# Kernel optimization log

Hardware: AMD Instinct MI355X
Metric: run time of the kernel (lower is better)

Reference implementation:

```python
import jax, jax.numpy as jnp
import numpy as np
from jax import lax


def _layernorm(x, g, b, eps=1e-5):
    mu = x.mean(-1, keepdims=True)
    var = ((x - mu) ** 2).mean(-1, keepdims=True)
    return (x - mu) * lax.rsqrt(var + eps) * g + b


def _conv1d(x, w, b):
    # x: (B, T, Cin), w: (K, Cin, Cout) -> (B, T, Cout), SAME padding
    return lax.conv_general_dilated(x, w, (1,), 'SAME',
                                    dimension_numbers=('NWC', 'WIO', 'NWC')) + b


def _gated(x, wf, bf, wg, bg):
    return jax.nn.relu(_conv1d(x, wf, bf)) * jax.nn.sigmoid(_conv1d(x, wg, bg))


def setup_inputs() -> dict:
    key = jax.random.key(0)
    ks = iter(jax.random.split(key, 32))
    B, T, F, H = 32, 1024, 64, 768
    ch = H // 3
    d = {'x': jax.random.normal(next(ks), (B, T, F), jnp.float32)}
    for k in (3, 5, 7):
        d[f'conv{k}_wf'] = jax.random.normal(next(ks), (k, F, ch), jnp.float32) * 0.05
        d[f'conv{k}_bf'] = jnp.zeros((ch,), jnp.float32)
        d[f'conv{k}_wg'] = jax.random.normal(next(ks), (k, F, ch), jnp.float32) * 0.05
        d[f'conv{k}_bg'] = jnp.zeros((ch,), jnp.float32)
    d['conv_ln_g'] = jnp.ones((H,), jnp.float32)
    d['conv_ln_b'] = jnp.zeros((H,), jnp.float32)
    for name in ('gqa_wq', 'gqa_wk', 'gqa_wv', 'gqa_wp'):
        d[name] = jax.random.normal(next(ks), (2, H, H), jnp.float32) * 0.02
    d['gqa_bp'] = jnp.zeros((2, H), jnp.float32)
    d['gqa_ln_g'] = jnp.ones((2, H), jnp.float32)
    d['gqa_ln_b'] = jnp.zeros((2, H), jnp.float32)
    d['proj_w'] = jax.random.normal(next(ks), (2 * H, H), jnp.float32) * 0.02
    d['proj_b'] = jnp.zeros((H,), jnp.float32)
    d['proj_ln_g'] = jnp.ones((H,), jnp.float32)
    d['proj_ln_b'] = jnp.zeros((H,), jnp.float32)
    return d


def _gqa(h, wq, wk, wv, wp, bp, ln_g, ln_b, n_groups=4):
    B, T, H = h.shape
    G, D = n_groups, H // n_groups
    scale = D ** -0.5
    Q = (h @ wq).reshape(B, T, G, D)
    K = (h @ wk).reshape(B, T, G, D)
    V = (h @ wv).reshape(B, T, G, D)
    attn = jax.nn.softmax(jnp.einsum('bqgd,bkgd->bgqk', Q, K) * scale, axis=-1)
    out = jnp.einsum('bgqk,bkgd->bqgd', attn, V).reshape(B, T, H)
    return _layernorm(h + out @ wp + bp, ln_g, ln_b)


def reference(x, conv3_wf, conv3_bf, conv3_wg, conv3_bg,
              conv5_wf, conv5_bf, conv5_wg, conv5_bg,
              conv7_wf, conv7_bf, conv7_wg, conv7_bg,
              conv_ln_g, conv_ln_b,
              gqa_wq, gqa_wk, gqa_wv, gqa_wp, gqa_bp, gqa_ln_g, gqa_ln_b,
              proj_w, proj_b, proj_ln_g, proj_ln_b):
    # Multi-scale gated conv front end (SAME padding -> all branches length T)
    o3 = _gated(x, conv3_wf, conv3_bf, conv3_wg, conv3_bg)
    o5 = _gated(x, conv5_wf, conv5_bf, conv5_wg, conv5_bg)
    o7 = _gated(x, conv7_wf, conv7_bf, conv7_wg, conv7_bg)
    h = _layernorm(jnp.concatenate([o3, o5, o7], axis=-1), conv_ln_g, conv_ln_b)
    # Two GQA blocks
    for i in range(2):
        h = _gqa(h, gqa_wq[i], gqa_wk[i], gqa_wv[i], gqa_wp[i],
                 gqa_bp[i], gqa_ln_g[i], gqa_ln_b[i])
    # mean + population-std pooling over time
    m = h.mean(axis=1)
    s = jnp.sqrt(((h - m[:, None, :]) ** 2).mean(axis=1))
    z = jnp.concatenate([m, s], axis=-1) @ proj_w + proj_b
    return jax.nn.relu(_layernorm(z, proj_ln_g, proj_ln_b))
```

## Files before the change

### kernel.cpp

```cpp
#include <hip/hip_runtime.h>
#include <hip/hip_bf16.h>


constexpr int Bb = 32, Tt = 1024, Ff = 64, Hh = 768, Gg = 4, Dd = 192;
constexpr float EPS = 1e-5f;
constexpr int WKMAX = 448;

typedef __attribute__((ext_vector_type(8))) short short8;
typedef __attribute__((ext_vector_type(4))) float floatx4;

__device__ __forceinline__ void async_copy16(const void* g, void* l) {
  __builtin_amdgcn_global_load_lds(
      (const __attribute__((address_space(1))) unsigned int*)g,
      (__attribute__((address_space(3))) unsigned int*)l, 16, 0, 0);
}

__device__ __forceinline__ short bf16s(float f) {
  __hip_bfloat16 h = __float2bfloat16(f);
  return *(short*)&h;
}

__device__ __forceinline__ unsigned int pack_bf16(float lo, float hi) {
  return (unsigned int)(unsigned short)bf16s(lo) |
         ((unsigned int)(unsigned short)bf16s(hi) << 16);
}

__device__ __forceinline__ float2 block_reduce2(float a, float b, float* tmp) {
  int lane = threadIdx.x & 63, wid = threadIdx.x >> 6;
#pragma unroll
  for (int off = 32; off > 0; off >>= 1) {
    a += __shfl_down(a, off);
    b += __shfl_down(b, off);
  }
  if (lane == 0) { tmp[wid] = a; tmp[4 + wid] = b; }
  __syncthreads();
  if (threadIdx.x == 0) {
    tmp[0] = tmp[0] + tmp[1] + tmp[2] + tmp[3];
    tmp[4] = tmp[4] + tmp[5] + tmp[6] + tmp[7];
  }
  __syncthreads();
  float2 r; r.x = tmp[0]; r.y = tmp[4];
  return r;
}

__global__ __launch_bounds__(256) void wt_cast_kernel(
    const float* __restrict__ wq, const float* __restrict__ wk,
    const float* __restrict__ wv, const float* __restrict__ wp,
    __hip_bfloat16* __restrict__ wt) {
  const int z = blockIdx.z;
  const int m = z & 3, i = z >> 2;
  const float* src =
      (m == 0 ? wq : m == 1 ? wk : m == 2 ? wv : wp) + (size_t)i * Hh * Hh;
  const float sc = (m == 0) ? 0.0721687836f : 1.f;
  __shared__ float tile[32][33];
  const int n0 = blockIdx.x * 32, k0 = blockIdx.y * 32;
  const int tx = threadIdx.x & 31, ty = threadIdx.x >> 5;
#pragma unroll
  for (int r = 0; r < 4; r++)
    tile[ty + 8 * r][tx] = src[(size_t)(k0 + ty + 8 * r) * Hh + n0 + tx];
  __syncthreads();
#pragma unroll
  for (int r = 0; r < 4; r++)
    wt[((size_t)z * Hh + n0 + ty + 8 * r) * Hh + k0 + tx] =
        __float2bfloat16(tile[tx][ty + 8 * r] * sc);
}

__global__ __launch_bounds__(256) void wcv_cast_kernel(
    const float* __restrict__ wf3, const float* __restrict__ wg3,
    const float* __restrict__ wf5, const float* __restrict__ wg5,
    const float* __restrict__ wf7, const float* __restrict__ wg7,
    __hip_bfloat16* __restrict__ wcv) {
  int idx = blockIdx.x * 256 + threadIdx.x;
  if (idx >= 3 * 512 * WKMAX) return;
  int j = idx / (512 * WKMAX);
  int rem = idx - j * 512 * WKMAX;
  int n = rem / WKMAX, k = rem % WKMAX;
  int Kw = 3 + 2 * j;
  float v = 0.f;
  if (k < Kw * 64) {
    const float* src = (n < 256) ? (j == 0 ? wf3 : j == 1 ? wf5 : wf7)
                                 : (j == 0 ? wg3 : j == 1 ? wg5 : wg7);
    v = src[(size_t)k * 256 + (n & 255)];
  }
  wcv[idx] = __float2bfloat16(v);
}

__global__ __launch_bounds__(256) void x_cast_kernel(
    const float* __restrict__ x, short* __restrict__ x16, int n8) {
  int idx = blockIdx.x * 256 + threadIdx.x;
  if (idx >= n8) return;
  const float4 a = ((const float4*)x)[idx * 2];
  const float4 b = ((const float4*)x)[idx * 2 + 1];
  short8 o;
  o[0] = bf16s(a.x); o[1] = bf16s(a.y); o[2] = bf16s(a.z); o[3] = bf16s(a.w);
  o[4] = bf16s(b.x); o[5] = bf16s(b.y); o[6] = bf16s(b.z); o[7] = bf16s(b.w);
  ((short8*)x16)[idx] = o;
}

__global__ __launch_bounds__(256) void conv_gemm_kernel(
    const short* __restrict__ x16, const short* __restrict__ wcv,
    short* __restrict__ yraw, int b0) {
  __shared__ __align__(16) short Asl[128 * 72];
  __shared__ __align__(16) short Bsl[128 * 72];
  const int t0 = blockIdx.x * 128, n0 = blockIdx.y * 128;
  const int bl = blockIdx.z / 3, j = blockIdx.z % 3;
  const int Kw = 3 + 2 * j, pad = j + 1;
  const int bglob = b0 + bl;
  const short* wb = wcv + (size_t)j * 512 * WKMAX;
  const int tid = threadIdx.x;
  const int lane = tid & 63;
  const int w = tid >> 6, wm = w >> 1, wn = w & 1;
  const int lm = lane & 15, quad = lane >> 4;

  floatx4 acc[4][4];
#pragma unroll
  for (int i = 0; i < 4; i++)
#pragma unroll
    for (int jj = 0; jj < 4; jj++) acc[i][jj] = (floatx4)0.f;

  for (int kk = 0; kk < Kw; kk++) {
    __syncthreads();
#pragma unroll
    for (int it = 0; it < 4; it++) {
      int s = it * 256 + tid;
      int row = s >> 3, c8 = s & 7;
      int t = t0 + row + kk - pad;
      short8 av = (short8)0;
      if (t >= 0 && t < Tt)
        av = *(const short8*)&x16[((size_t)bglob * Tt + t) * Ff + c8 * 8];
      *(short8*)&Asl[row * 72 + c8 * 8] = av;
      short8 bv = *(const short8*)&wb[(size_t)(n0 + row) * WKMAX + kk * 64 +
                                      c8 * 8];
      *(short8*)&Bsl[row * 72 + c8 * 8] = bv;
    }
    __syncthreads();
#pragma unroll
    for (int ks = 0; ks < 2; ks++) {
      short8 a[4], b[4];
#pragma unroll
      for (int i = 0; i < 4; i++)
        a[i] = *(const short8*)&Asl[(wm * 64 + i * 16 + lm) * 72 + ks * 32 +
                                    quad * 8];
#pragma unroll
      for (int jj = 0; jj < 4; jj++)
        b[jj] = *(const short8*)&Bsl[(wn * 64 + jj * 16 + lm) * 72 + ks * 32 +
                                     quad * 8];
#pragma unroll
      for (int i = 0; i < 4; i++)
#pragma unroll
        for (int jj = 0; jj < 4; jj++)
          acc[i][jj] = __builtin_amdgcn_mfma_f32_16x16x32_bf16(a[i], b[jj],
                                                               acc[i][jj],
                                                               0, 0, 0);
    }
  }

  const int rbase = quad * 4;
#pragma unroll
  for (int i = 0; i < 4; i++)
#pragma unroll
    for (int jj = 0; jj < 4; jj++) {
      int mrow = t0 + wm * 64 + i * 16 + rbase;
      int ncol = n0 + wn * 64 + jj * 16 + lm;
#pragma unroll
      for (int r = 0; r < 4; r++)
        yraw[((size_t)bl * Tt + mrow + r) * 1536 + j * 512 + ncol] =
            bf16s(acc[i][jj][r]);
    }
}

__global__ __launch_bounds__(256) void gate_ln_kernel(
    const short* __restrict__ yraw, __hip_bfloat16* __restrict__ h16,
    const float* __restrict__ bf3, const float* __restrict__ bg3,
    const float* __restrict__ bf5, const float* __restrict__ bg5,
    const float* __restrict__ bf7, const float* __restrict__ bg7,
    const float* __restrict__ g, const float* __restrict__ bt) {
  __shared__ float red[8];
  const size_t row = blockIdx.x;
  float v[3], s = 0.f, ss = 0.f;
#pragma unroll
  for (int jj = 0; jj < 3; jj++) {
    int c = threadIdx.x + jj * 256;
    int br = c >> 8, cc = c & 255;
    const float* bfp = br == 0 ? bf3 : br == 1 ? bf5 : bf7;
    const float* bgp = br == 0 ? bg3 : br == 1 ? bg5 : bg7;
    __hip_bfloat16 rf = *(const __hip_bfloat16*)&yraw[row * 1536 + br * 512 + cc];
    __hip_bfloat16 rg =
        *(const __hip_bfloat16*)&yraw[row * 1536 + br * 512 + 256 + cc];
    float f = __bfloat162float(rf) + bfp[cc];
    float gt = __bfloat162float(rg) + bgp[cc];
    float a = f > 0.f ? f : 0.f;
    float t = a * (1.f / (1.f + __expf(-gt)));
    v[jj] = t; s += t; ss += t * t;
  }
  float2 r = block_reduce2(s, ss, red);
  float mu = r.x * (1.f / Hh);
  float var = r.y * (1.f / Hh) - mu * mu;
  float rs = rsqrtf(var + EPS);
#pragma unroll
  for (int jj = 0; jj < 3; jj++) {
    int c = threadIdx.x + jj * 256;
    float o = (v[jj] - mu) * rs * g[c] + bt[c];
    h16[row * Hh + c] = __float2bfloat16(o);
  }
}

__global__ __launch_bounds__(256) void res_ln_kernel(
    __hip_bfloat16* __restrict__ h16, const __hip_bfloat16* __restrict__ y,
    const float* __restrict__ bp, const float* __restrict__ g,
    const float* __restrict__ bt) {
  __shared__ float red[8];
  const size_t row = blockIdx.x;
  float v[3], s = 0.f, ss = 0.f;
#pragma unroll
  for (int jj = 0; jj < 3; jj++) {
    int c = threadIdx.x + jj * 256;
    float t = __bfloat162float(h16[row * Hh + c]) +
              __bfloat162float(y[row * Hh + c]) + bp[c];
    v[jj] = t; s += t; ss += t * t;
  }
  float2 r = block_reduce2(s, ss, red);
  float mu = r.x * (1.f / Hh);
  float var = r.y * (1.f / Hh) - mu * mu;
  float rs = rsqrtf(var + EPS);
#pragma unroll
  for (int jj = 0; jj < 3; jj++) {
    int c = threadIdx.x + jj * 256;
    float o = (v[jj] - mu) * rs * g[c] + bt[c];
    h16[row * Hh + c] = __float2bfloat16(o);
  }
}

template <int MODE>
__global__ __launch_bounds__(512, 2) void gemm_8ph(
    const short* __restrict__ A, const short* __restrict__ Bt,
    short* __restrict__ out_q, short* __restrict__ out_k,
    short* __restrict__ out_v) {
  constexpr int K = 768;
  constexpr int NT = K / 32;
  constexpr int NB = (MODE == 0) ? 9 : 3;
  __shared__ __align__(16) short lds[4][16384];

  const int nwg = gridDim.x;
  const int qq = nwg >> 3, rr = nwg & 7;
  const int xcd = blockIdx.x & 7, bidx = blockIdx.x >> 3;
  const int swz =
      (xcd < rr ? xcd * (qq + 1) : rr * (qq + 1) + (xcd - rr) * qq) + bidx;
  const int nb = swz % NB, mb = swz / NB;
  const int n0 = nb * 256, m0 = mb * 256;

  const int tid = threadIdx.x;
  const int lane = tid & 63, w = tid >> 6;
  const int lm = lane & 15, quad = lane >> 4;
  const int wm = w >> 2, wn = w & 3;

  const short* sA[2];
  const short* sB[2];
  int dst[2];
#pragma unroll
  for (int li = 0; li < 2; li++) {
    int l = li * 512 + tid;
    int reg = l >> 6, cs = l & 63;
    int cs2 = cs ^ (((cs >> 5) & 1) << 1);
    int row = (reg << 4) + (cs2 >> 2);
    int col = (cs2 & 3) << 3;
    sA[li] = A + (size_t)(m0 + row) * K + col;
    sB[li] = Bt + (size_t)(n0 + row) * K + col;
    dst[li] = l * 8;
  }

#define STAGE8(kt, ring)                                   \
  {                                                        \
    const int _o = (kt) * 32;                              \
    async_copy16(sA[0] + _o, &lds[ring][dst[0]]);          \
    async_copy16(sB[0] + _o, &lds[ring][8192 + dst[0]]);   \
    async_copy16(sA[1] + _o, &lds[ring][dst[1]]);          \
    async_copy16(sB[1] + _o, &lds[ring][8192 + dst[1]]);   \
  }

  const int lane_sh = (lm * 32 + quad * 8) ^ ((lm >> 3) << 4);

  floatx4 acc[8][4];
#pragma unroll
  for (int i = 0; i < 8; i++)
#pragma unroll
    for (int j = 0; j < 4; j++) acc[i][j] = (floatx4)0.f;

  STAGE8(0, 0);
  STAGE8(1, 1);
  STAGE8(2, 2);
  asm volatile("s_waitcnt vmcnt(8)" ::: "memory");
  asm volatile("s_barrier" ::: "memory");
  __builtin_amdgcn_sched_barrier(0);

  for (int t = 0; t < NT; t++) {
    const int ring = t & 3;
    if (t + 3 < NT) STAGE8(t + 3, (t + 3) & 3);

    short8 a[8], b[4];
#pragma unroll
    for (int i = 0; i < 8; i++)
      a[i] = *(const short8*)&lds[ring][(wm * 8 + i) * 512 + lane_sh];
#pragma unroll
    for (int j = 0; j < 4; j++)
      b[j] = *(const short8*)&lds[ring][8192 + (wn * 4 + j) * 512 + lane_sh];

    __builtin_amdgcn_s_setprio(1);
#pragma unroll
    for (int i = 0; i < 8; i++)
#pragma unroll
      for (int j = 0; j < 4; j++)
        acc[i][j] = __builtin_amdgcn_mfma_f32_16x16x32_bf16(a[i], b[j],
                                                            acc[i][j],
                                                            0, 0, 0);
    __builtin_amdgcn_s_setprio(0);

    if (t < NT - 1) {
      if (t < NT - 3)
        asm volatile("s_waitcnt vmcnt(8)" ::: "memory");
      else if (t == NT - 3)
        asm volatile("s_waitcnt vmcnt(4)" ::: "memory");
      else
        asm volatile("s_waitcnt vmcnt(0)" ::: "memory");
      asm volatile("s_barrier" ::: "memory");
      __builtin_amdgcn_sched_barrier(0);
    }
  }
#undef STAGE8

  const int rbase = quad * 4;
  if (MODE == 1) {
#pragma unroll
    for (int i = 0; i < 8; i++) {
      const int mrow = m0 + wm * 128 + i * 16 + rbase;
#pragma unroll
      for (int j = 0; j < 4; j++) {
        const int ncol = n0 + wn * 64 + j * 16 + lm;
#pragma unroll
        for (int r = 0; r < 4; r++)
          out_q[(size_t)(mrow + r) * Hh + ncol] = bf16s(acc[i][j][r]);
      }
    }
  } else {
    const int which = nb / 3;
    const int nbase = (nb % 3) * 256;
#pragma unroll
    for (int i = 0; i < 8; i++) {
      const int mrow = m0 + wm * 128 + i * 16 + rbase;
#pragma unroll
      for (int j = 0; j < 4; j++) {
        const int nl = nbase + wn * 64 + j * 16 + lm;
        if (which == 0) {
#pragma unroll
          for (int r = 0; r < 4; r++)
            out_q[(size_t)(mrow + r) * Hh + nl] = bf16s(acc[i][j][r]);
        } else if (which == 1) {
#pragma unroll
          for (int r = 0; r < 4; r++)
            out_k[(size_t)(mrow + r) * Hh + nl] = bf16s(acc[i][j][r]);
        } else {
          const int bL = mrow >> 10, ttok = mrow & 1023;
          const int g = nl / Dd, d = nl % Dd;
          short4 sv;
          sv.x = bf16s(acc[i][j][0]); sv.y = bf16s(acc[i][j][1]);
          sv.z = bf16s(acc[i][j][2]); sv.w = bf16s(acc[i][j][3]);
          *(short4*)&out_v[(((size_t)bL * Gg + g) * Dd + d) * Tt + ttok] = sv;
        }
      }
    }
  }
}

__global__ __launch_bounds__(256, 2) void attn_mfma(
    const short* __restrict__ q16, const short* __restrict__ k16,
    const short* __restrict__ vt16, short* __restrict__ o16, int chunk4) {
  const int bg = blockIdx.x % chunk4;
  const int qb = blockIdx.x / chunk4;
  const int b = bg >> 2, g = bg & 3;
  const int q0 = qb * 128;
  const int tid = threadIdx.x;
  const int w = tid >> 6, lane = tid & 63, lm = lane & 15, quad = lane >> 4;

  __shared__ __align__(16) short Ks[2][32 * 200];
  __shared__ __align__(16) short Vt[2][208 * 32];
  constexpr int VBUF = 208 * 32;

  for (int e = tid; e < 2 * 16 * 32; e += 256) {
    int buf = e >> 9;
    int r = e & 511;
    Vt[buf][192 * 32 + r] = (r < 32) ? (short)0x3F80 : (short)0;
  }

  short8 qf[2][6];
#pragma unroll
  for (int mt = 0; mt < 2; mt++)
#pragma unroll
    for (int ks = 0; ks < 6; ks++) {
      int tok = b * Tt + q0 + w * 32 + mt * 16 + lm;
      qf[mt][ks] = *(const short8*)&q16[(size_t)tok * Hh + g * Dd + ks * 32 +
                                        quad * 8];
    }

  floatx4 Oa[2][13];
#pragma unroll
  for (int mt = 0; mt < 2; mt++)
#pragma unroll
    for (int n = 0; n < 13; n++) Oa[mt][n] = (floatx4)0.f;

  int krow[3], kcs[3];
  const short* kgp[3];
  const short* vgp[3];
  short* vld[3];
#pragma unroll
  for (int it = 0; it < 3; it++) {
    int s = it * 256 + tid;
    krow[it] = s / 24; kcs[it] = s - krow[it] * 24;
    kgp[it] = &k16[(size_t)(b * Tt + krow[it]) * Hh + g * Dd + kcs[it] * 8];
    vgp[it] = &vt16[(((size_t)b * Gg + g) * Dd + (s >> 2)) * Tt + (s & 3) * 8];
    vld[it] = (short*)&Vt[0][0] + (size_t)s * 8;
  }

  short8 kvK[3];
#pragma unroll
  for (int it = 0; it < 3; it++) kvK[it] = *(const short8*)kgp[it];
#pragma unroll
  for (int it = 0; it < 3; it++)
    *(short8*)&Ks[0][krow[it] * 200 + kcs[it] * 8] = kvK[it];
#pragma unroll
  for (int it = 0; it < 3; it++)
    kvK[it] = *(const short8*)(kgp[it] + (size_t)32 * Hh);
#pragma unroll
  for (int it = 0; it < 3; it++) async_copy16(vgp[it], vld[it]);

  for (int i = 0; i < 32; i++) {
    const int ib = i & 1;
    __syncthreads();

    if (i + 1 < 32) {
#pragma unroll
      for (int it = 0; it < 3; it++)
        *(short8*)&Ks[ib ^ 1][krow[it] * 200 + kcs[it] * 8] = kvK[it];
      const int vo = (i + 1) * 32;
#pragma unroll
      for (int it = 0; it < 3; it++)
        async_copy16(vgp[it] + vo, vld[it] + (ib ^ 1) * VBUF);
      if (i + 2 < 32) {
        const size_t ko = (size_t)(i + 2) * 32 * Hh;
#pragma unroll
        for (int it = 0; it < 3; it++)
          kvK[it] = *(const short8*)(kgp[it] + ko);
      }
    }

    floatx4 st[2][2];
#pragma unroll
    for (int mt = 0; mt < 2; mt++)
#pragma unroll
      for (int jj = 0; jj < 2; jj++) st[mt][jj] = (floatx4)0.f;
#pragma unroll
    for (int ks = 0; ks < 6; ks++) {
      short8 k0 = *(const short8*)&Ks[ib][lm * 200 + ks * 32 + quad * 8];
      short8 k1 = *(const short8*)&Ks[ib][(16 + lm) * 200 + ks * 32 + quad * 8];
      st[0][0] = __builtin_amdgcn_mfma_f32_16x16x32_bf16(k0, qf[0][ks], st[0][0], 0, 0, 0);
      st[0][1] = __builtin_amdgcn_mfma_f32_16x16x32_bf16(k1, qf[0][ks], st[0][1], 0, 0, 0);
      st[1][0] = __builtin_amdgcn_mfma_f32_16x16x32_bf16(k0, qf[1][ks], st[1][0], 0, 0, 0);
      st[1][1] = __builtin_amdgcn_mfma_f32_16x16x32_bf16(k1, qf[1][ks], st[1][1], 0, 0, 0);
    }

    short8 ptf[2];
#pragma unroll
    for (int mt = 0; mt < 2; mt++) {
      float p[2][4];
#pragma unroll
      for (int jj = 0; jj < 2; jj++)
#pragma unroll
        for (int r = 0; r < 4; r++) p[jj][r] = __expf(st[mt][jj][r]);

      int pk00 = (int)pack_bf16(p[0][0], p[0][1]);
      int pk01 = (int)pack_bf16(p[0][2], p[0][3]);
      int pk10 = (int)pack_bf16(p[1][0], p[1][1]);
      int pk11 = (int)pack_bf16(p[1][2], p[1][3]);
      int srcA = ((quad & 1) << 5) + lm;
      int srcB = srcA + 16;
      int a0 = __shfl(pk00, srcA), a1 = __shfl(pk01, srcA);
      int a2 = __shfl(pk00, srcB), a3 = __shfl(pk01, srcB);
      int b0 = __shfl(pk10, srcA), b1 = __shfl(pk11, srcA);
      int b2 = __shfl(pk10, srcB), b3 = __shfl(pk11, srcB);
      bool hi = quad >= 2;
      union { int u[4]; short8 v; } pu;
      pu.u[0] = hi ? b0 : a0;
      pu.u[1] = hi ? b1 : a1;
      pu.u[2] = hi ? b2 : a2;
      pu.u[3] = hi ? b3 : a3;
      ptf[mt] = pu.v;
    }

#pragma unroll
    for (int n = 0; n < 13; n++) {
      short8 vf = *(const short8*)&Vt[ib][(n * 16 + lm) * 32 + quad * 8];
      Oa[0][n] = __builtin_amdgcn_mfma_f32_16x16x32_bf16(vf, ptf[0], Oa[0][n], 0, 0, 0);
      Oa[1][n] = __builtin_amdgcn_mfma_f32_16x16x32_bf16(vf, ptf[1], Oa[1][n], 0, 0, 0);
    }
  }

#pragma unroll
  for (int mt = 0; mt < 2; mt++) {
    float lval = __shfl(Oa[mt][12][0], lm);
    float inv = 1.f / lval;
    int tok = b * Tt + q0 + w * 32 + mt * 16 + lm;
#pragma unroll
    for (int n = 0; n < 12; n++) {
      short4 sv;
      sv.x = bf16s(Oa[mt][n][0] * inv);
      sv.y = bf16s(Oa[mt][n][1] * inv);
      sv.z = bf16s(Oa[mt][n][2] * inv);
      sv.w = bf16s(Oa[mt][n][3] * inv);
      *(short4*)&o16[(size_t)tok * Hh + g * Dd + n * 16 + quad * 4] = sv;
    }
  }
}

__global__ __launch_bounds__(256) void pool_stage1(
    const __hip_bfloat16* __restrict__ h16, float* __restrict__ ppart,
    int b0) {
  int idx = blockIdx.x * 256 + threadIdx.x;
  int seg = blockIdx.y;
  int bl = idx / Hh, c = idx % Hh;
  float s = 0.f, ss = 0.f;
  const __hip_bfloat16* hp = &h16[((size_t)bl * Tt + seg * 128) * Hh + c];
  for (int t = 0; t < 128; t++) {
    float v = __bfloat162float(hp[(size_t)t * Hh]);
    s += v; ss += v * v;
  }
  float* o = &ppart[(((size_t)(b0 + bl) * 8 + seg) * 2) * Hh + c];
  o[0] = s;
  o[Hh] = ss;
}

__global__ __launch_bounds__(256) void pool_stage2(
    const float* __restrict__ ppart, float* __restrict__ pool) {
  int idx = blockIdx.x * 256 + threadIdx.x;
  int b = idx / Hh, c = idx % Hh;
  float s = 0.f, ss = 0.f;
#pragma unroll
  for (int seg = 0; seg < 8; seg++) {
    const float* o = &ppart[(((size_t)b * 8 + seg) * 2) * Hh + c];
    s += o[0]; ss += o[Hh];
  }
  float mu = s * (1.f / Tt);
  float var = ss * (1.f / Tt) - mu * mu;
  pool[(size_t)b * 1536 + c] = mu;
  pool[(size_t)b * 1536 + 768 + c] = sqrtf(fmaxf(var, 0.f));
}

__global__ __launch_bounds__(256) void final_partial(
    const float* __restrict__ pool, const float* __restrict__ pw,
    float* __restrict__ part) {
  const int n = blockIdx.x * 256 + threadIdx.x;
  const int bg = blockIdx.y * 4;
  const int ks = blockIdx.z, k0 = ks * 192;
  __shared__ float ms[4][192];
  for (int e = threadIdx.x; e < 4 * 192; e += 256) {
    int bb = e / 192, kk = e % 192;
    ms[bb][kk] = pool[(size_t)(bg + bb) * 1536 + k0 + kk];
  }
  __syncthreads();
  float a0 = 0.f, a1 = 0.f, a2 = 0.f, a3 = 0.f;
  for (int kk = 0; kk < 192; kk++) {
    float wv = pw[(size_t)(k0 + kk) * Hh + n];
    a0 = fmaf(ms[0][kk], wv, a0);
    a1 = fmaf(ms[1][kk], wv, a1);
    a2 = fmaf(ms[2][kk], wv, a2);
    a3 = fmaf(ms[3][kk], wv, a3);
  }
  part[((size_t)ks * Bb + bg + 0) * Hh + n] = a0;
  part[((size_t)ks * Bb + bg + 1) * Hh + n] = a1;
  part[((size_t)ks * Bb + bg + 2) * Hh + n] = a2;
  part[((size_t)ks * Bb + bg + 3) * Hh + n] = a3;
}

__global__ __launch_bounds__(256) void final_stage2(
    const float* __restrict__ part, const float* __restrict__ pb,
    const float* __restrict__ g, const float* __restrict__ bt,
    float* __restrict__ out) {
  __shared__ float red[8];
  const int b = blockIdx.x;
  float v[3], s = 0.f, ss = 0.f;
#pragma unroll
  for (int jj = 0; jj < 3; jj++) {
    int n = threadIdx.x + jj * 256;
    float a = pb[n];
#pragma unroll
    for (int ks = 0; ks < 8; ks++) a += part[((size_t)ks * Bb + b) * Hh + n];
    v[jj] = a; s += a; ss += a * a;
  }
  float2 r = block_reduce2(s, ss, red);
  float mu = r.x * (1.f / Hh);
  float var = r.y * (1.f / Hh) - mu * mu;
  float rs = rsqrtf(var + EPS);
#pragma unroll
  for (int jj = 0; jj < 3; jj++) {
    int n = threadIdx.x + jj * 256;
    float o = (v[jj] - mu) * rs * g[n] + bt[n];
    out[(size_t)b * Hh + n] = o > 0.f ? o : 0.f;
  }
}

extern "C" void kernel_launch(void* const* d_in, const int* in_sizes, int n_in,
                              void* d_out, int out_size, void* d_ws,
                              size_t ws_size, hipStream_t stream) {
  (void)in_sizes; (void)n_in; (void)out_size;
  const float* x = (const float*)d_in[0];
  const float* cw[3][4];
  for (int j = 0; j < 3; j++)
    for (int p2 = 0; p2 < 4; p2++) cw[j][p2] = (const float*)d_in[1 + j * 4 + p2];
  const float* conv_ln_g = (const float*)d_in[13];
  const float* conv_ln_b = (const float*)d_in[14];
  const float* wq = (const float*)d_in[15];
  const float* wk = (const float*)d_in[16];
  const float* wv = (const float*)d_in[17];
  const float* wp = (const float*)d_in[18];
  const float* bp = (const float*)d_in[19];
  const float* lng = (const float*)d_in[20];
  const float* lnb = (const float*)d_in[21];
  const float* proj_w = (const float*)d_in[22];
  const float* proj_b = (const float*)d_in[23];
  const float* proj_ln_g = (const float*)d_in[24];
  const float* proj_ln_b = (const float*)d_in[25];
  float* out = (float*)d_out;

  const size_t perb = (size_t)Tt * Hh;
  const size_t fixedB = 8ull * Hh * Hh * 2 + 3ull * 512 * WKMAX * 2 +
                        (size_t)Bb * Tt * Ff * 2 + (size_t)Bb * 2 * Hh * 4 +
                        (size_t)Bb * 8 * 2 * Hh * 4 + 8ull * Bb * Hh * 4;
  int chunk = Bb;
  while (chunk > 1 && 8ull * perb * chunk + fixedB > ws_size) chunk >>= 1;

  const size_t crow = perb * (size_t)chunk;
  char* p = (char*)d_ws;
  __hip_bfloat16* h16 = (__hip_bfloat16*)p;  p += crow * 2;
  short* q16 = (short*)p;            p += crow * 2;
  short* k16 = (short*)p;            p += crow * 2;
  short* v16t = (short*)p;           p += crow * 2;
  short* yraw16 = q16;
  short* y16 = k16;
  __hip_bfloat16* wt = (__hip_bfloat16*)p;   p += 8ull * Hh * Hh * 2;
  __hip_bfloat16* wcv = (__hip_bfloat16*)p;  p += 3ull * 512 * WKMAX * 2;
  short* x16 = (short*)p;            p += (size_t)Bb * Tt * Ff * 2;
  float* pool = (float*)p;           p += (size_t)Bb * 2 * Hh * 4;
  float* ppart = (float*)p;          p += (size_t)Bb * 8 * 2 * Hh * 4;
  float* fpart = (float*)p;

  wt_cast_kernel<<<dim3(24, 24, 8), 256, 0, stream>>>(wq, wk, wv, wp, wt);
  wcv_cast_kernel<<<(3 * 512 * WKMAX + 255) / 256, 256, 0, stream>>>(
      cw[0][0], cw[0][2], cw[1][0], cw[1][2], cw[2][0], cw[2][2], wcv);
  x_cast_kernel<<<(Bb * Tt * Ff / 8 + 255) / 256, 256, 0, stream>>>(
      x, x16, Bb * Tt * Ff / 8);

  const short* wts = (const short*)wt;

  for (int b0 = 0; b0 < Bb; b0 += chunk) {
    const int M = chunk * Tt;

    conv_gemm_kernel<<<dim3(Tt / 128, 4, chunk * 3), 256, 0, stream>>>(
        x16, (const short*)wcv, yraw16, b0);
    gate_ln_kernel<<<M, 256, 0, stream>>>(
        yraw16, h16, cw[0][1], cw[0][3], cw[1][1], cw[1][3], cw[2][1],
        cw[2][3], conv_ln_g, conv_ln_b);

    for (int i = 0; i < 2; i++) {
      const short* wqkv = wts + (size_t)(i * 4) * Hh * Hh;
      const short* wtp = wts + (size_t)(i * 4 + 3) * Hh * Hh;
      gemm_8ph<0><<<dim3(9 * (M / 256)), 512, 0, stream>>>(
          (const short*)h16, wqkv, q16, k16, v16t);
      attn_mfma<<<dim3(chunk * Gg * (Tt / 128)), 256, 0, stream>>>(
          q16, k16, v16t, q16, chunk * Gg);
      gemm_8ph<1><<<dim3(3 * (M / 256)), 512, 0, stream>>>(
          q16, wtp, y16, nullptr, nullptr);
      res_ln_kernel<<<M, 256, 0, stream>>>(h16, (const __hip_bfloat16*)y16,
                                           bp + (size_t)i * Hh,
                                           lng + (size_t)i * Hh,
                                           lnb + (size_t)i * Hh);
    }

    pool_stage1<<<dim3((chunk * Hh) / 256, 8), 256, 0, stream>>>(h16, ppart,
                                                                 b0);
  }

  pool_stage2<<<(Bb * Hh) / 256, 256, 0, stream>>>(ppart, pool);
  final_partial<<<dim3(3, 8, 8), 256, 0, stream>>>(pool, proj_w, fpart);
  final_stage2<<<Bb, 256, 0, stream>>>(fpart, proj_b, proj_ln_g, proj_ln_b,
                                       out);
}
```

Measured before the change: 934.2 us.

## Software-pipeline LDS fragment loads across the barrier in GEMM main loop

Restructures the GEMM K-loop so the first half of the next tile's A/B fragments are read from LDS right after the barrier, while the second half of the current tile's MFMAs run. The loop is unrolled by two with ping-pong register sets. The goal is to hide LDS read latency behind MFMA work instead of stalling at the start of each iteration. This raises register pressure and assumes NT is even.

```diff
diff --git a/kernel.cpp b/kernel.cpp
--- a/kernel.cpp
+++ b/kernel.cpp
@@ -280,6 +280,11 @@
 
   const int lane_sh = (lm * 32 + quad * 8) ^ ((lm >> 3) << 4);
 
+#define FRAG_A(ring, i) \
+  (*(const short8*)&lds[ring][(wm * 8 + (i)) * 512 + lane_sh])
+#define FRAG_B(ring, j) \
+  (*(const short8*)&lds[ring][8192 + (wn * 4 + (j)) * 512 + lane_sh])
+
   floatx4 acc[8][4];
 #pragma unroll
   for (int i = 0; i < 8; i++)
@@ -293,40 +298,78 @@
   asm volatile("s_barrier" ::: "memory");
   __builtin_amdgcn_sched_barrier(0);
 
-  for (int t = 0; t < NT; t++) {
-    const int ring = t & 3;
-    if (t + 3 < NT) STAGE8(t + 3, (t + 3) & 3);
-
-    short8 a[8], b[4];
-#pragma unroll
-    for (int i = 0; i < 8; i++)
-      a[i] = *(const short8*)&lds[ring][(wm * 8 + i) * 512 + lane_sh];
-#pragma unroll
-    for (int j = 0; j < 4; j++)
-      b[j] = *(const short8*)&lds[ring][8192 + (wn * 4 + j) * 512 + lane_sh];
-
-    __builtin_amdgcn_s_setprio(1);
-#pragma unroll
-    for (int i = 0; i < 8; i++)
-#pragma unroll
-      for (int j = 0; j < 4; j++)
-        acc[i][j] = __builtin_amdgcn_mfma_f32_16x16x32_bf16(a[i], b[j],
-                                                            acc[i][j],
-                                                            0, 0, 0);
-    __builtin_amdgcn_s_setprio(0);
-
-    if (t < NT - 1) {
-      if (t < NT - 3)
-        asm volatile("s_waitcnt vmcnt(8)" ::: "memory");
-      else if (t == NT - 3)
-        asm volatile("s_waitcnt vmcnt(4)" ::: "memory");
-      else
-        asm volatile("s_waitcnt vmcnt(0)" ::: "memory");
-      asm volatile("s_barrier" ::: "memory");
-      __builtin_amdgcn_sched_barrier(0);
-    }
-  }
+  short8 bc0[4], al0[4], bc1[4], al1[4];
+  bc0[0] = FRAG_B(0, 0); bc0[1] = FRAG_B(0, 1);
+  bc0[2] = FRAG_B(0, 2); bc0[3] = FRAG_B(0, 3);
+  al0[0] = FRAG_A(0, 0); al0[1] = FRAG_A(0, 1);
+  al0[2] = FRAG_A(0, 2); al0[3] = FRAG_A(0, 3);
+
+#define ITER(t, bC, aL, bN, aN)                                              \
+  {                                                                          \
+    const int ring = (t) & 3, nring = ((t) + 1) & 3;                         \
+    if ((t) + 3 < NT) STAGE8((t) + 3, ((t) + 3) & 3);                        \
+    short8 ah0 = FRAG_A(ring, 4), ah1 = FRAG_A(ring, 5),                     \
+           ah2 = FRAG_A(ring, 6), ah3 = FRAG_A(ring, 7);                     \
+    __builtin_amdgcn_s_setprio(1);                                           \
+    acc[0][0] = __builtin_amdgcn_mfma_f32_16x16x32_bf16(aL[0], bC[0], acc[0][0], 0, 0, 0); \
+    acc[0][1] = __builtin_amdgcn_mfma_f32_16x16x32_bf16(aL[0], bC[1], acc[0][1], 0, 0, 0); \
+    acc[0][2] = __builtin_amdgcn_mfma_f32_16x16x32_bf16(aL[0], bC[2], acc[0][2], 0, 0, 0); \
+    acc[0][3] = __builtin_amdgcn_mfma_f32_16x16x32_bf16(aL[0], bC[3], acc[0][3], 0, 0, 0); \
+    acc[1][0] = __builtin_amdgcn_mfma_f32_16x16x32_bf16(aL[1], bC[0], acc[1][0], 0, 0, 0); \
+    acc[1][1] = __builtin_amdgcn_mfma_f32_16x16x32_bf16(aL[1], bC[1], acc[1][1], 0, 0, 0); \
+    acc[1][2] = __builtin_amdgcn_mfma_f32_16x16x32_bf16(aL[1], bC[2], acc[1][2], 0, 0, 0); \
+    acc[1][3] = __builtin_amdgcn_mfma_f32_16x16x32_bf16(aL[1], bC[3], acc[1][3], 0, 0, 0); \
+    acc[2][0] = __builtin_amdgcn_mfma_f32_16x16x32_bf16(aL[2], bC[0], acc[2][0], 0, 0, 0); \
+    acc[2][1] = __builtin_amdgcn_mfma_f32_16x16x32_bf16(aL[2], bC[1], acc[2][1], 0, 0, 0); \
+    acc[2][2] = __builtin_amdgcn_mfma_f32_16x16x32_bf16(aL[2], bC[2], acc[2][2], 0, 0, 0); \
+    acc[2][3] = __builtin_amdgcn_mfma_f32_16x16x32_bf16(aL[2], bC[3], acc[2][3], 0, 0, 0); \
+    acc[3][0] = __builtin_amdgcn_mfma_f32_16x16x32_bf16(aL[3], bC[0], acc[3][0], 0, 0, 0); \
+    acc[3][1] = __builtin_amdgcn_mfma_f32_16x16x32_bf16(aL[3], bC[1], acc[3][1], 0, 0, 0); \
+    acc[3][2] = __builtin_amdgcn_mfma_f32_16x16x32_bf16(aL[3], bC[2], acc[3][2], 0, 0, 0); \
+    acc[3][3] = __builtin_amdgcn_mfma_f32_16x16x32_bf16(aL[3], bC[3], acc[3][3], 0, 0, 0); \
+    __builtin_amdgcn_s_setprio(0);                                           \
+    if ((t) < NT - 1) {                                                      \
+      if ((t) < NT - 3)                                                      \
+        asm volatile("s_waitcnt vmcnt(8)" ::: "memory");                     \
+      else if ((t) == NT - 3)                                                \
+        asm volatile("s_waitcnt vmcnt(4)" ::: "memory");                     \
+      else                                                                   \
+        asm volatile("s_waitcnt vmcnt(0)" ::: "memory");                     \
+      asm volatile("s_barrier" ::: "memory");                                \
+      __builtin_amdgcn_sched_barrier(0);                                     \
+      bN[0] = FRAG_B(nring, 0); bN[1] = FRAG_B(nring, 1);                    \
+      bN[2] = FRAG_B(nring, 2); bN[3] = FRAG_B(nring, 3);                    \
+      aN[0] = FRAG_A(nring, 0); aN[1] = FRAG_A(nring, 1);                    \
+      aN[2] = FRAG_A(nring, 2); aN[3] = FRAG_A(nring, 3);                    \
+    }                                                                        \
+    __builtin_amdgcn_s_setprio(1);                                           \
+    acc[4][0] = __builtin_amdgcn_mfma_f32_16x16x32_bf16(ah0, bC[0], acc[4][0], 0, 0, 0); \
+    acc[4][1] = __builtin_amdgcn_mfma_f32_16x16x32_bf16(ah0, bC[1], acc[4][1], 0, 0, 0); \
+    acc[4][2] = __builtin_amdgcn_mfma_f32_16x16x32_bf16(ah0, bC[2], acc[4][2], 0, 0, 0); \
+    acc[4][3] = __builtin_amdgcn_mfma_f32_16x16x32_bf16(ah0, bC[3], acc[4][3], 0, 0, 0); \
+    acc[5][0] = __builtin_amdgcn_mfma_f32_16x16x32_bf16(ah1, bC[0], acc[5][0], 0, 0, 0); \
+    acc[5][1] = __builtin_amdgcn_mfma_f32_16x16x32_bf16(ah1, bC[1], acc[5][1], 0, 0, 0); \
+    acc[5][2] = __builtin_amdgcn_mfma_f32_16x16x32_bf16(ah1, bC[2], acc[5][2], 0, 0, 0); \
+    acc[5][3] = __builtin_amdgcn_mfma_f32_16x16x32_bf16(ah1, bC[3], acc[5][3], 0, 0, 0); \
+    acc[6][0] = __builtin_amdgcn_mfma_f32_16x16x32_bf16(ah2, bC[0], acc[6][0], 0, 0, 0); \
+    acc[6][1] = __builtin_amdgcn_mfma_f32_16x16x32_bf16(ah2, bC[1], acc[6][1], 0, 0, 0); \
+    acc[6][2] = __builtin_amdgcn_mfma_f32_16x16x32_bf16(ah2, bC[2], acc[6][2], 0, 0, 0); \
+    acc[6][3] = __builtin_amdgcn_mfma_f32_16x16x32_bf16(ah2, bC[3], acc[6][3], 0, 0, 0); \
+    acc[7][0] = __builtin_amdgcn_mfma_f32_16x16x32_bf16(ah3, bC[0], acc[7][0], 0, 0, 0); \
+    acc[7][1] = __builtin_amdgcn_mfma_f32_16x16x32_bf16(ah3, bC[1], acc[7][1], 0, 0, 0); \
+    acc[7][2] = __builtin_amdgcn_mfma_f32_16x16x32_bf16(ah3, bC[2], acc[7][2], 0, 0, 0); \
+    acc[7][3] = __builtin_amdgcn_mfma_f32_16x16x32_bf16(ah3, bC[3], acc[7][3], 0, 0, 0); \
+    __builtin_amdgcn_s_setprio(0);                                           \
+  }
+
+  for (int t = 0; t < NT; t += 2) {
+    ITER(t, bc0, al0, bc1, al1);
+    ITER(t + 1, bc1, al1, bc0, al0);
+  }
+#undef ITER
 #undef STAGE8
+#undef FRAG_A
+#undef FRAG_B
 
   const int rbase = quad * 4;
   if (MODE == 1) {
```

New measurement: 905.2 us. 1.03x faster.

## Restructure GEMM main loop into 8-phase ping-pong schedule with K=64 tiles

Applied to the files above, without the earlier changes.

Replaces the 4-deep ring of K=32 tiles in the bf16 MFMA GEMM with a double buffer of K=64 tiles. Each tile is split into four quarter phases: LDS fragment loads, async global-to-LDS staging of the next tile's quarter, and an MFMA block, with barriers between them. The aim is to interleave memory traffic with MFMA work at a finer grain and reduce the register pressure of the fragments. The extra barriers per iteration and tighter vmcnt bookkeeping add sync overhead and risk stalls or hazards if the waits are mis-sized.

```diff
diff --git a/kernel.cpp b/kernel.cpp
--- a/kernel.cpp
+++ b/kernel.cpp
@@ -237,9 +237,10 @@
     short* __restrict__ out_q, short* __restrict__ out_k,
     short* __restrict__ out_v) {
   constexpr int K = 768;
-  constexpr int NT = K / 32;
+  constexpr int NT = K / 64;
+  constexpr int NI = NT / 2;
   constexpr int NB = (MODE == 0) ? 9 : 3;
-  __shared__ __align__(16) short lds[4][16384];
+  __shared__ __align__(16) short lds[65536];
 
   const int nwg = gridDim.x;
   const int qq = nwg >> 3, rr = nwg & 7;
@@ -254,31 +255,32 @@
   const int lm = lane & 15, quad = lane >> 4;
   const int wm = w >> 2, wn = w & 3;
 
-  const short* sA[2];
-  const short* sB[2];
-  int dst[2];
+  int srow[2], scol[2], dst8[2];
 #pragma unroll
   for (int li = 0; li < 2; li++) {
-    int l = li * 512 + tid;
-    int reg = l >> 6, cs = l & 63;
+    int c = li * 512 + tid;
+    int ks = c >> 9, rem = c & 511;
+    int reg = rem >> 6, cs = rem & 63;
     int cs2 = cs ^ (((cs >> 5) & 1) << 1);
-    int row = (reg << 4) + (cs2 >> 2);
-    int col = (cs2 & 3) << 3;
-    sA[li] = A + (size_t)(m0 + row) * K + col;
-    sB[li] = Bt + (size_t)(n0 + row) * K + col;
-    dst[li] = l * 8;
-  }
-
-#define STAGE8(kt, ring)                                   \
-  {                                                        \
-    const int _o = (kt) * 32;                              \
-    async_copy16(sA[0] + _o, &lds[ring][dst[0]]);          \
-    async_copy16(sB[0] + _o, &lds[ring][8192 + dst[0]]);   \
-    async_copy16(sA[1] + _o, &lds[ring][dst[1]]);          \
-    async_copy16(sB[1] + _o, &lds[ring][8192 + dst[1]]);   \
+    srow[li] = (reg << 4) + (cs2 >> 2);
+    scol[li] = ks * 32 + (cs2 & 3) * 8;
+    dst8[li] = ks * 8192 + rem * 8;
+  }
+
+#define STG(T, ISB, H)                                                     \
+  {                                                                        \
+    _Pragma("unroll") for (int li = 0; li < 2; li++) {                     \
+      const short* sp = ((ISB) ? Bt : A) +                                 \
+          (size_t)((((ISB) ? n0 : m0) + (H) * 128 + srow[li])) * K +       \
+          (T) * 64 + scol[li];                                             \
+      async_copy16(sp, &lds[((T) & 1) * 32768 + (ISB) * 16384 +            \
+                            (H) * 4096 + dst8[li]]);                       \
+    }                                                                      \
   }
 
   const int lane_sh = (lm * 32 + quad * 8) ^ ((lm >> 3) << 4);
+  const int abase = wm * 8;
+  const int bbase = wn * 4;
 
   floatx4 acc[8][4];
 #pragma unroll
@@ -286,47 +288,78 @@
 #pragma unroll
     for (int j = 0; j < 4; j++) acc[i][j] = (floatx4)0.f;
 
-  STAGE8(0, 0);
-  STAGE8(1, 1);
-  STAGE8(2, 2);
-  asm volatile("s_waitcnt vmcnt(8)" ::: "memory");
-  asm volatile("s_barrier" ::: "memory");
-  __builtin_amdgcn_sched_barrier(0);
-
-  for (int t = 0; t < NT; t++) {
-    const int ring = t & 3;
-    if (t + 3 < NT) STAGE8(t + 3, (t + 3) & 3);
-
-    short8 a[8], b[4];
-#pragma unroll
-    for (int i = 0; i < 8; i++)
-      a[i] = *(const short8*)&lds[ring][(wm * 8 + i) * 512 + lane_sh];
-#pragma unroll
-    for (int j = 0; j < 4; j++)
-      b[j] = *(const short8*)&lds[ring][8192 + (wn * 4 + j) * 512 + lane_sh];
-
-    __builtin_amdgcn_s_setprio(1);
-#pragma unroll
-    for (int i = 0; i < 8; i++)
-#pragma unroll
-      for (int j = 0; j < 4; j++)
-        acc[i][j] = __builtin_amdgcn_mfma_f32_16x16x32_bf16(a[i], b[j],
-                                                            acc[i][j],
-                                                            0, 0, 0);
-    __builtin_amdgcn_s_setprio(0);
-
-    if (t < NT - 1) {
-      if (t < NT - 3)
-        asm volatile("s_waitcnt vmcnt(8)" ::: "memory");
-      else if (t == NT - 3)
-        asm volatile("s_waitcnt vmcnt(4)" ::: "memory");
-      else
-        asm volatile("s_waitcnt vmcnt(0)" ::: "memory");
-      asm volatile("s_barrier" ::: "memory");
-      __builtin_amdgcn_sched_barrier(0);
-    }
-  }
-#undef STAGE8
+  short8 aF[4][2], bF[2][2];
+
+#define LDA(CB, MH)                                                        \
+  _Pragma("unroll") for (int mi = 0; mi < 4; mi++)                         \
+    _Pragma("unroll") for (int ks = 0; ks < 2; ks++)                       \
+      aF[mi][ks] = *(const short8*)&lds[(CB) + ks * 8192 +                 \
+          (abase + (MH) * 4 + mi) * 512 + lane_sh];
+#define LDB(CB, NH)                                                        \
+  _Pragma("unroll") for (int nj = 0; nj < 2; nj++)                         \
+    _Pragma("unroll") for (int ks = 0; ks < 2; ks++)                       \
+      bF[nj][ks] = *(const short8*)&lds[(CB) + 16384 + ks * 8192 +         \
+          (bbase + (NH) * 2 + nj) * 512 + lane_sh];
+#define MM(MH, NH)                                                         \
+  __builtin_amdgcn_s_setprio(1);                                           \
+  _Pragma("unroll") for (int mi = 0; mi < 4; mi++)                         \
+    _Pragma("unroll") for (int nj = 0; nj < 2; nj++)                       \
+      _Pragma("unroll") for (int ks = 0; ks < 2; ks++)                     \
+        acc[(MH) * 4 + mi][(NH) * 2 + nj] =                                \
+            __builtin_amdgcn_mfma_f32_16x16x32_bf16(                       \
+                aF[mi][ks], bF[nj][ks],                                    \
+                acc[(MH) * 4 + mi][(NH) * 2 + nj], 0, 0, 0);               \
+  __builtin_amdgcn_s_setprio(0);
+#define BARRIER asm volatile("s_barrier" ::: "memory")
+#define WAITV2 asm volatile("s_waitcnt vmcnt(2)" ::: "memory")
+#define WAITV0 asm volatile("s_waitcnt vmcnt(0)" ::: "memory")
+
+  STG(0, 0, 0); STG(0, 0, 1); STG(0, 1, 0); STG(0, 1, 1);
+  WAITV0;
+  BARRIER;
+
+#pragma unroll
+  for (int i = 0; i < NI; i++) {
+    const int T0 = 2 * i;
+    LDA(0, 0); LDB(0, 0);
+    STG(T0 + 1, 0, 1);
+    if (i == 0) STG(1, 0, 0);
+    BARRIER; MM(0, 0); BARRIER;
+    LDB(0, 1);
+    STG(T0 + 1, 1, 0);
+    BARRIER; MM(0, 1); BARRIER;
+    LDA(0, 1); LDB(0, 0);
+    STG(T0 + 1, 1, 1);
+    BARRIER; MM(1, 0); BARRIER;
+    LDB(0, 1);
+    if (T0 + 2 < NT) STG(T0 + 2, 0, 0);
+    BARRIER; MM(1, 1);
+    if (i < NI - 1) { WAITV2; } else { WAITV0; }
+    BARRIER;
+    LDA(32768, 0); LDB(32768, 0);
+    if (T0 + 2 < NT) STG(T0 + 2, 0, 1);
+    BARRIER; MM(0, 0); BARRIER;
+    LDB(32768, 1);
+    if (T0 + 2 < NT) STG(T0 + 2, 1, 0);
+    BARRIER; MM(0, 1); BARRIER;
+    LDA(32768, 1); LDB(32768, 0);
+    if (T0 + 2 < NT) STG(T0 + 2, 1, 1);
+    BARRIER; MM(1, 0); BARRIER;
+    LDB(32768, 1);
+    if (T0 + 3 < NT) STG(T0 + 3, 0, 0);
+    BARRIER; MM(1, 1);
+    if (i < NI - 1) {
+      WAITV2;
+      BARRIER;
+    }
+  }
+#undef STG
+#undef LDA
+#undef LDB
+#undef MM
+#undef BARRIER
+#undef WAITV2
+#undef WAITV0
 
   const int rbase = quad * 4;
   if (MODE == 1) {
```

After: 933.1 us. Within noise of the previous version (-0.1%).
